# Kernel optimization log

Measured on AMD Instinct MI355X. Metric: run time of the kernel, lower is better.

Reference implementation:

```python
import jax, jax.numpy as jnp
import numpy as np

B, T, C, H = 4, 1024, 2048, 16
D = C // H  # head dim = 128
ALPHA_Q, BETA_Q = -128, 127


def _quant_params(w):
    # symmetric range per tensor, as in get_symmetric_range/get_tensor_quantization_parameters
    beta = float(np.abs(w).max())
    alpha = -beta
    s = (beta - alpha) / (BETA_Q - ALPHA_Q)
    z = int((beta * ALPHA_Q - alpha * BETA_Q) / (beta - alpha))
    return s, z


def _quantize(w, s, z):
    return np.clip(np.round(w / s + z), ALPHA_Q, BETA_Q).astype(np.int8)


def setup_inputs() -> dict:
    key = jax.random.key(0)
    x = jax.random.normal(key, (B, T, C), dtype=jnp.float32)
    rng = np.random.default_rng(0)
    # fp32 master weights (GPT init scale), then quantize per-tensor symmetric int8
    params = {
        'w_attn': rng.normal(0.0, 0.02, (3 * C, C)).astype(np.float32),
        'b_attn': rng.normal(0.0, 0.02, (3 * C,)).astype(np.float32),
        'w_proj': rng.normal(0.0, 0.02, (C, C)).astype(np.float32),
        'b_proj': rng.normal(0.0, 0.02, (C,)).astype(np.float32),
    }
    out = {'x': x}
    for name, arr in params.items():
        s, z = _quant_params(arr)
        out[name + '_q'] = jnp.asarray(_quantize(arr, s, z))
        out['s_' + name] = jnp.float32(s)
        out['z_' + name] = z  # python int, zero-point constant
    return out


def _dequant(wq, s, z):
    # dequantize_tensor: s * (int8 -> int32 - z) -> float32
    return s * (wq.astype(jnp.int32) - z).astype(jnp.float32)


def reference(x, w_attn_q, s_w_attn, z_w_attn, b_attn_q, s_b_attn, z_b_attn,
              w_proj_q, s_w_proj, z_w_proj, b_proj_q, s_b_proj, z_b_proj):
    wa = _dequant(w_attn_q, s_w_attn, z_w_attn)   # [3C, C]
    ba = _dequant(b_attn_q, s_b_attn, z_b_attn)   # [3C]
    wp = _dequant(w_proj_q, s_w_proj, z_w_proj)   # [C, C]
    bp = _dequant(b_proj_q, s_b_proj, z_b_proj)   # [C]

    qkv = jnp.einsum('btc,oc->bto', x, wa) + ba   # [B,T,3C]
    q, k, v = jnp.split(qkv, 3, axis=-1)
    # [B,T,C] -> [B,H,T,D]
    q = q.reshape(B, T, H, D).transpose(0, 2, 1, 3)
    k = k.reshape(B, T, H, D).transpose(0, 2, 1, 3)
    v = v.reshape(B, T, H, D).transpose(0, 2, 1, 3)

    scale = 1.0 / jnp.sqrt(jnp.float32(D))
    scores = jnp.einsum('bhqd,bhkd->bhqk', q, k) * scale  # [B,H,T,T]
    causal = jnp.tril(jnp.ones((T, T), dtype=bool))
    scores = jnp.where(causal, scores, jnp.finfo(scores.dtype).min)
    att = jax.nn.softmax(scores, axis=-1)
    y = jnp.einsum('bhqk,bhkd->bhqd', att, v)      # [B,H,T,D]
    y = y.transpose(0, 2, 1, 3).reshape(B, T, C)

    return jnp.einsum('btc,oc->bto', y, wp) + bp   # [B,T,C]
```

## Files before the change

### kernel.cpp

```cpp
#include <hip/hip_runtime.h>
#include <stdint.h>
#include <math.h>

typedef unsigned short u16;
typedef __attribute__((ext_vector_type(4))) float f32x4;
typedef __attribute__((ext_vector_type(4))) int i32x4;
typedef __attribute__((ext_vector_type(8))) short bf16x8;

__device__ __forceinline__ u16 f2bf(float f) {
  uint32_t u = __float_as_uint(f);
  u += 0x7FFFu + ((u >> 16) & 1u);
  return (u16)(u >> 16);
}

__device__ __forceinline__ void async16(const void* g, void* l) {
  __builtin_amdgcn_global_load_lds(
      (const __attribute__((address_space(1))) void*)g,
      (__attribute__((address_space(3))) void*)l, 16, 0, 0);
}

__global__ void absmax_x(const float4* __restrict__ x, unsigned* __restrict__ amax, int n4) {
  int i = blockIdx.x * 256 + threadIdx.x;
  float m = 0.f;
  for (; i < n4; i += gridDim.x * 256) {
    float4 v = x[i];
    m = fmaxf(m, fmaxf(fmaxf(fabsf(v.x), fabsf(v.y)), fmaxf(fabsf(v.z), fabsf(v.w))));
  }
#pragma unroll
  for (int s = 1; s < 64; s <<= 1) m = fmaxf(m, __shfl_xor(m, s));
  if ((threadIdx.x & 63) == 0) atomicMax(amax, __float_as_uint(m));
}

__global__ void quant_x(const float4* __restrict__ x, char4* __restrict__ o,
                        const unsigned* __restrict__ amax, int n4) {
  int i = blockIdx.x * 256 + threadIdx.x;
  if (i >= n4) return;
  const float inv = 127.0f / __uint_as_float(amax[0]);
  float4 v = x[i];
  char4 r;
  r.x = (char)__float2int_rn(v.x * inv);
  r.y = (char)__float2int_rn(v.y * inv);
  r.z = (char)__float2int_rn(v.z * inv);
  r.w = (char)__float2int_rn(v.w * inv);
  o[i] = r;
}

__global__ void dequant_w8(const int4* __restrict__ q, char4* __restrict__ o, int n4,
                           const int* __restrict__ z) {
  int i = blockIdx.x * 256 + threadIdx.x;
  if (i >= n4) return;
  const int zv = z[0];
  int4 v = q[i];
  char4 r;
  r.x = (char)(v.x - zv); r.y = (char)(v.y - zv);
  r.z = (char)(v.z - zv); r.w = (char)(v.w - zv);
  o[i] = r;
}

__global__ void dequant4(const int4* __restrict__ q, ushort4* __restrict__ o, int n4,
                         const float* __restrict__ s, const int* __restrict__ z) {
  int i = blockIdx.x * 256 + threadIdx.x;
  if (i >= n4) return;
  const float sv = s[0];
  const int zv = z[0];
  int4 v = q[i];
  ushort4 r;
  r.x = f2bf(sv * (float)(v.x - zv));
  r.y = f2bf(sv * (float)(v.y - zv));
  r.z = f2bf(sv * (float)(v.z - zv));
  r.w = f2bf(sv * (float)(v.w - zv));
  o[i] = r;
}

__global__ __launch_bounds__(256, 2) void gemm_i8_qkv(
    const char* __restrict__ A, const char* __restrict__ B, int K,
    const float* __restrict__ sw, const unsigned* __restrict__ amax,
    const int* __restrict__ bq, const float* __restrict__ bs, const int* __restrict__ bz,
    u16* __restrict__ qb, u16* __restrict__ kb, u16* __restrict__ vT) {
  __shared__ uint8_t sA[16384];
  __shared__ uint8_t sB[16384];
  const int tid = threadIdx.x;
  const int wave = tid >> 6, lane = tid & 63;
  const int quad = lane >> 4, l16 = lane & 15;
  const int wm = wave >> 1, wn = wave & 1;
  const int Mb = blockIdx.y << 7, Nb = blockIdx.x << 7;

  const char* ag[4];
  const char* bg[4];
  int lo[4];
#pragma unroll
  for (int i = 0; i < 4; ++i) {
    int row = wave * 32 + i * 8 + (lane >> 3);
    int c = (lane & 7) ^ (row & 7);
    ag[i] = A + (size_t)(Mb + row) * K + c * 16;
    bg[i] = B + (size_t)(Nb + row) * K + c * 16;
    lo[i] = wave * 4096 + i * 1024 + lane * 16;
  }

  i32x4 acc[4][4] = {};

  for (int kk = 0; kk < K; kk += 128) {
    __syncthreads();
#pragma unroll
    for (int i = 0; i < 4; ++i) {
      async16(ag[i] + kk, sA + lo[i]);
      async16(bg[i] + kk, sB + lo[i]);
    }
    __syncthreads();
#pragma unroll
    for (int ks = 0; ks < 2; ++ks) {
      i32x4 af[4], bfr[4];
#pragma unroll
      for (int t = 0; t < 4; ++t) {
        int m = wm * 64 + t * 16 + l16;
        af[t] = *(const i32x4*)(sA + m * 128 + ((((ks << 2) + quad) ^ (m & 7)) << 4));
        int n = wn * 64 + t * 16 + l16;
        bfr[t] = *(const i32x4*)(sB + n * 128 + ((((ks << 2) + quad) ^ (n & 7)) << 4));
      }
#pragma unroll
      for (int mt = 0; mt < 4; ++mt)
#pragma unroll
        for (int nt = 0; nt < 4; ++nt)
          acc[mt][nt] = __builtin_amdgcn_mfma_i32_16x16x64_i8(af[mt], bfr[nt], acc[mt][nt], 0, 0, 0);
    }
  }

  const float sv = sw[0] * (__uint_as_float(amax[0]) / 127.0f);
  const float sbv = bs[0];
  const int zbv = bz[0];
#pragma unroll
  for (int nt = 0; nt < 4; ++nt) {
    const int o = Nb + wn * 64 + nt * 16 + l16;
    const float bias = sbv * (float)(bq[o] - zbv);
    const int which = o >> 11;
    const int cc = o & 2047;
    const int h = cc >> 7, d = cc & 127;
#pragma unroll
    for (int mt = 0; mt < 4; ++mt) {
      const int m0 = Mb + wm * 64 + mt * 16 + quad * 4;
      const int bi = m0 >> 10, t0 = m0 & 1023;
      const size_t bhx = (size_t)bi * 16 + h;
      if (which == 2) {
        ushort4 pv;
        pv.x = f2bf((float)acc[mt][nt][0] * sv + bias);
        pv.y = f2bf((float)acc[mt][nt][1] * sv + bias);
        pv.z = f2bf((float)acc[mt][nt][2] * sv + bias);
        pv.w = f2bf((float)acc[mt][nt][3] * sv + bias);
        *(ushort4*)(vT + (bhx * 128 + d) * 1024 + t0) = pv;
      } else {
        u16* dst = (which == 0 ? qb : kb) + (bhx * 1024 + t0) * 128 + d;
#pragma unroll
        for (int r = 0; r < 4; ++r) dst[r * 128] = f2bf((float)acc[mt][nt][r] * sv + bias);
      }
    }
  }
}

__global__ __launch_bounds__(256, 2) void gemm_bt_out(
    const u16* __restrict__ A, const u16* __restrict__ B, int K, int N,
    const int* __restrict__ bq, const float* __restrict__ bs, const int* __restrict__ bz,
    float* __restrict__ out) {
  __shared__ uint8_t sA[16384];
  __shared__ uint8_t sB[16384];
  const int tid = threadIdx.x;
  const int wave = tid >> 6, lane = tid & 63;
  const int quad = lane >> 4, l16 = lane & 15;
  const int wm = wave >> 1, wn = wave & 1;
  const int Mb = blockIdx.y << 7, Nb = blockIdx.x << 7;

  const u16* ag[4];
  const u16* bg[4];
  int lo[4];
#pragma unroll
  for (int i = 0; i < 4; ++i) {
    int row = wave * 32 + i * 8 + (lane >> 3);
    int c = (lane & 7) ^ (row & 7);
    ag[i] = A + (size_t)(Mb + row) * K + c * 8;
    bg[i] = B + (size_t)(Nb + row) * K + c * 8;
    lo[i] = wave * 4096 + i * 1024 + lane * 16;
  }

  f32x4 acc[4][4] = {};

  for (int kk = 0; kk < K; kk += 64) {
    __syncthreads();
#pragma unroll
    for (int i = 0; i < 4; ++i) {
      async16(ag[i] + kk, sA + lo[i]);
      async16(bg[i] + kk, sB + lo[i]);
    }
    __syncthreads();
#pragma unroll
    for (int ks = 0; ks < 2; ++ks) {
      bf16x8 af[4], bfr[4];
#pragma unroll
      for (int t = 0; t < 4; ++t) {
        int m = wm * 64 + t * 16 + l16;
        af[t] = *(const bf16x8*)(sA + m * 128 + ((((ks << 2) + quad) ^ (m & 7)) << 4));
        int n = wn * 64 + t * 16 + l16;
        bfr[t] = *(const bf16x8*)(sB + n * 128 + ((((ks << 2) + quad) ^ (n & 7)) << 4));
      }
#pragma unroll
      for (int mt = 0; mt < 4; ++mt)
#pragma unroll
        for (int nt = 0; nt < 4; ++nt)
          acc[mt][nt] = __builtin_amdgcn_mfma_f32_16x16x32_bf16(af[mt], bfr[nt], acc[mt][nt], 0, 0, 0);
    }
  }

  const float sbv = bs[0];
  const int zbv = bz[0];
#pragma unroll
  for (int nt = 0; nt < 4; ++nt) {
    const int o = Nb + wn * 64 + nt * 16 + l16;
    const float bias = sbv * (float)(bq[o] - zbv);
#pragma unroll
    for (int mt = 0; mt < 4; ++mt) {
      const int m0 = Mb + wm * 64 + mt * 16 + quad * 4;
#pragma unroll
      for (int r = 0; r < 4; ++r)
        out[(size_t)(m0 + r) * N + o] = acc[mt][nt][r] + bias;
    }
  }
}

__global__ __launch_bounds__(256, 2) void attn_fwd(
    const u16* __restrict__ qg, const u16* __restrict__ kg,
    const u16* __restrict__ vg, u16* __restrict__ yb) {
  __shared__ uint8_t smem[49152];
  uint8_t* sK = smem;
  uint8_t* sV = smem + 16384;
  uint8_t* sP = smem + 32768;
  const int tid = threadIdx.x;
  const int wave = tid >> 6, lane = tid & 63;
  const int quad = lane >> 4, l16 = lane & 15;
  const int bh = blockIdx.x;
  const int y = blockIdx.y;
  const int qi = (y < 4) ? (7 - y) : (y - 4);
  const int qbase = qi << 7;
  const size_t base = (size_t)bh << 17;
  const u16* Q = qg + base;
  const u16* Kp = kg + base;
  const u16* Vp = vg + base;

#pragma unroll
  for (int i = 0; i < 8; ++i) {
    int off = wave * 8192 + i * 1024;
    int row = (off >> 8) + quad;
    int c = l16 ^ (row & 15);
    async16(Q + (size_t)(qbase + row) * 128 + c * 8, smem + off + lane * 16);
  }
  __syncthreads();
  bf16x8 qf[2][4];
#pragma unroll
  for (int mi = 0; mi < 2; ++mi)
#pragma unroll
    for (int ks = 0; ks < 4; ++ks) {
      int m = wave * 32 + mi * 16 + l16;
      qf[mi][ks] = *(const bf16x8*)(smem + m * 256 + ((((ks << 2) + quad) ^ (m & 15)) << 4));
    }

  f32x4 accO[2][8] = {};
  float lacc[2][4] = {};

  const float scale = 0.088388347648318447f;
  const int jmax = 2 * qi + 1;

  for (int j = 0; j <= jmax; ++j) {
    const int tb = j << 6;
    __syncthreads();
#pragma unroll
    for (int i = 0; i < 4; ++i) {
      int off = wave * 4096 + i * 1024;
      int rowk = (off >> 8) + quad;
      int ck = l16 ^ (rowk & 15);
      async16(Kp + (size_t)(tb + rowk) * 128 + ck * 8, sK + off + lane * 16);
      int rowd = (off >> 7) + (lane >> 3);
      int cv = (lane & 7) ^ (rowd & 7);
      async16(Vp + (size_t)rowd * 1024 + tb + cv * 8, sV + off + lane * 16);
    }
    __syncthreads();

    f32x4 sc[2][4] = {};
#pragma unroll
    for (int ks = 0; ks < 4; ++ks) {
      bf16x8 kf[4];
#pragma unroll
      for (int ni = 0; ni < 4; ++ni) {
        int n = ni * 16 + l16;
        kf[ni] = *(const bf16x8*)(sK + n * 256 + ((((ks << 2) + quad) ^ (n & 15)) << 4));
      }
#pragma unroll
      for (int mi = 0; mi < 2; ++mi)
#pragma unroll
        for (int ni = 0; ni < 4; ++ni)
          sc[mi][ni] = __builtin_amdgcn_mfma_f32_16x16x32_bf16(qf[mi][ks], kf[ni], sc[mi][ni], 0, 0, 0);
    }

    const bool needmask = (tb + 63) > qbase;
#pragma unroll
    for (int mi = 0; mi < 2; ++mi) {
      const int row0 = qbase + wave * 32 + mi * 16 + quad * 4;
#pragma unroll
      for (int ni = 0; ni < 4; ++ni) {
        const int col = tb + ni * 16 + l16;
#pragma unroll
        for (int r = 0; r < 4; ++r) {
          float s = sc[mi][ni][r] * scale;
          if (needmask && col > row0 + r) s = -INFINITY;
          float p = __expf(s);
          sc[mi][ni][r] = p;
          lacc[mi][r] += p;
        }
      }
    }

#pragma unroll
    for (int mi = 0; mi < 2; ++mi)
#pragma unroll
      for (int ni = 0; ni < 4; ++ni)
#pragma unroll
        for (int r = 0; r < 4; ++r) {
          int qr = wave * 32 + mi * 16 + quad * 4 + r;
          int kc = ni * 16 + l16;
          *(u16*)(sP + qr * 128 + (((kc >> 3) ^ (qr & 7)) << 4) + (kc & 7) * 2) =
              f2bf(sc[mi][ni][r]);
        }

#pragma unroll
    for (int ks = 0; ks < 2; ++ks) {
      bf16x8 pf[2], vf[8];
#pragma unroll
      for (int mi = 0; mi < 2; ++mi) {
        int m = wave * 32 + mi * 16 + l16;
        pf[mi] = *(const bf16x8*)(sP + m * 128 + ((((ks << 2) + quad) ^ (m & 7)) << 4));
      }
#pragma unroll
      for (int ni = 0; ni < 8; ++ni) {
        int n = ni * 16 + l16;
        vf[ni] = *(const bf16x8*)(sV + n * 128 + ((((ks << 2) + quad) ^ (n & 7)) << 4));
      }
#pragma unroll
      for (int mi = 0; mi < 2; ++mi)
#pragma unroll
        for (int ni = 0; ni < 8; ++ni)
          accO[mi][ni] = __builtin_amdgcn_mfma_f32_16x16x32_bf16(pf[mi], vf[ni], accO[mi][ni], 0, 0, 0);
    }
  }

  const int b = bh >> 4, h = bh & 15;
#pragma unroll
  for (int mi = 0; mi < 2; ++mi) {
    float inv[4];
#pragma unroll
    for (int r = 0; r < 4; ++r) {
      float l = lacc[mi][r];
#pragma unroll
      for (int x = 1; x < 16; x <<= 1) l += __shfl_xor(l, x);
      inv[r] = 1.0f / l;
    }
#pragma unroll
    for (int ni = 0; ni < 8; ++ni)
#pragma unroll
      for (int r = 0; r < 4; ++r) {
        int row = qbase + wave * 32 + mi * 16 + quad * 4 + r;
        int col = (h << 7) + ni * 16 + l16;
        yb[((size_t)(b * 1024 + row) << 11) + col] = f2bf(accO[mi][ni][r] * inv[r]);
      }
  }
}

extern "C" void kernel_launch(void* const* d_in, const int* in_sizes, int n_in,
                              void* d_out, int out_size, void* d_ws, size_t ws_size,
                              hipStream_t stream) {
  const float* x = (const float*)d_in[0];
  const int* waq = (const int*)d_in[1];
  const float* s_wa = (const float*)d_in[2];
  const int* z_wa = (const int*)d_in[3];
  const int* baq = (const int*)d_in[4];
  const float* s_ba = (const float*)d_in[5];
  const int* z_ba = (const int*)d_in[6];
  const int* wpq = (const int*)d_in[7];
  const float* s_wp = (const float*)d_in[8];
  const int* z_wp = (const int*)d_in[9];
  const int* bpq = (const int*)d_in[10];
  const float* s_bp = (const float*)d_in[11];
  const int* z_bp = (const int*)d_in[12];

  char* ws = (char*)d_ws;
  char* xq    = ws + 0;
  char* wa8   = ws + 8388608;
  u16* wp_bf  = (u16*)(ws + 20971520);
  u16* qb     = (u16*)(ws + 29360128);
  u16* kb     = (u16*)(ws + 46137344);
  u16* vT     = (u16*)(ws + 62914560);
  u16* yb     = (u16*)(ws + 79691776);
  unsigned* amax = (unsigned*)(ws + 96468992);

  hipMemsetAsync(amax, 0, 4, stream);
  absmax_x<<<1024, 256, 0, stream>>>((const float4*)x, amax, 2097152);
  quant_x<<<8192, 256, 0, stream>>>((const float4*)x, (char4*)xq, amax, 2097152);
  dequant_w8<<<12288, 256, 0, stream>>>((const int4*)waq, (char4*)wa8, 3145728, z_wa);
  dequant4<<<4096, 256, 0, stream>>>((const int4*)wpq, (ushort4*)wp_bf, 1048576, s_wp, z_wp);

  gemm_i8_qkv<<<dim3(48, 32), 256, 0, stream>>>(xq, wa8, 2048, s_wa, amax,
                                                baq, s_ba, z_ba, qb, kb, vT);

  attn_fwd<<<dim3(64, 8), 256, 0, stream>>>(qb, kb, vT, yb);

  gemm_bt_out<<<dim3(16, 32), 256, 0, stream>>>(yb, wp_bf, 2048, 2048,
                                                bpq, s_bp, z_bp, (float*)d_out);
}
```

Baseline: 338.9 us.

## Rewrite int8 QKV GEMM as 256x256 double-buffered ping-pong pipeline with block swizzle

```diff
diff --git a/kernel.cpp b/kernel.cpp
--- a/kernel.cpp
+++ b/kernel.cpp
@@ -72,85 +72,160 @@
   o[i] = r;
 }
 
-__global__ __launch_bounds__(256, 2) void gemm_i8_qkv(
+
+#define STAGE_A(Q, C, KK, SL) do {                                           \
+    const int row_ = (C)*128 + (Q)*64 + (tid>>3);                            \
+    const int ch_ = (tid&7) ^ (row_&7);                                      \
+    async16(A + (size_t)(Mb + row_)*2048 + (KK) + ch_*16,                    \
+            sA + (SL)*32768 + (C)*16384 + (Q)*8192 + tid*16);                \
+  } while(0)
+
+#define STAGE_B(S, C, KK, SL) do {                                           \
+    const int t8_ = tid & 255, hi_ = tid >> 8;                               \
+    const int row_ = (C)*128 + hi_*64 + (S)*32 + (t8_>>3);                   \
+    const int ch_ = (tid&7) ^ (row_&7);                                      \
+    async16(B + (size_t)(Nb + row_)*2048 + (KK) + ch_*16,                    \
+            sB + (SL)*32768 + (C)*16384 + hi_*8192 + (S)*4096 + t8_*16);     \
+  } while(0)
+
+#define LDA(DST, MQ, SL)                                                     \
+  _Pragma("unroll")                                                          \
+  for (int mp_ = 0; mp_ < 4; ++mp_)                                          \
+    _Pragma("unroll")                                                        \
+    for (int ks_ = 0; ks_ < 2; ++ks_) {                                      \
+      const int r_ = wm*128 + (MQ)*64 + mp_*16 + l16;                        \
+      DST[mp_][ks_] = *(const i32x4*)(sA + (SL)*32768 + r_*128 +             \
+                                      ((((ks_<<2)+quad) ^ (r_&7)) << 4));    \
+    }
+
+#define LDB(DST, NQ, SL)                                                     \
+  _Pragma("unroll")                                                          \
+  for (int np_ = 0; np_ < 2; ++np_)                                          \
+    _Pragma("unroll")                                                        \
+    for (int ks_ = 0; ks_ < 2; ++ks_) {                                      \
+      const int r_ = wn*64 + (NQ)*32 + np_*16 + l16;                         \
+      DST[np_][ks_] = *(const i32x4*)(sB + (SL)*32768 + r_*128 +             \
+                                      ((((ks_<<2)+quad) ^ (r_&7)) << 4));    \
+    }
+
+#define MFMA_QUAD(AF, BF, MQ, NQ)                                            \
+  _Pragma("unroll")                                                          \
+  for (int ks_ = 0; ks_ < 2; ++ks_)                                          \
+    _Pragma("unroll")                                                        \
+    for (int mp_ = 0; mp_ < 4; ++mp_)                                        \
+      _Pragma("unroll")                                                      \
+      for (int np_ = 0; np_ < 2; ++np_)                                      \
+        acc[(MQ)*4+mp_][(NQ)*2+np_] = __builtin_amdgcn_mfma_i32_16x16x64_i8( \
+            AF[mp_][ks_], BF[np_][ks_], acc[(MQ)*4+mp_][(NQ)*2+np_], 0, 0, 0);
+
+#define BARRIER __builtin_amdgcn_s_barrier()
+#define WAIT_LGKM0 do { asm volatile("s_waitcnt lgkmcnt(0)" ::: "memory");   \
+                        __builtin_amdgcn_sched_barrier(0); } while(0)
+#define WAIT_VM8 asm volatile("s_waitcnt vmcnt(8)" ::: "memory")
+
+#define ITER(CUR, NXT, KK2) do {                                             \
+                                                                \
+    STAGE_A(0,0,KK2,CUR); STAGE_A(0,1,KK2,CUR);                              \
+    LDB(b1, 1, CUR);                                                         \
+    BARRIER; WAIT_LGKM0;                                                     \
+    __builtin_amdgcn_s_setprio(1);                                           \
+    MFMA_QUAD(a0, b0, 0, 0);                                                 \
+    __builtin_amdgcn_s_setprio(0);                                           \
+    BARRIER;                                                                 \
+                                                                \
+    LDA(a1, 1, CUR);                                                         \
+    BARRIER; WAIT_LGKM0;                                                     \
+    __builtin_amdgcn_s_setprio(1);                                           \
+    MFMA_QUAD(a0, b1, 0, 1);                                                 \
+    __builtin_amdgcn_s_setprio(0);                                           \
+    BARRIER;                                                                 \
+                                                                \
+    STAGE_A(1,0,KK2,CUR); STAGE_A(1,1,KK2,CUR);                              \
+    STAGE_B(0,0,KK2,CUR); STAGE_B(0,1,KK2,CUR);                              \
+    BARRIER; WAIT_LGKM0;                                                     \
+    __builtin_amdgcn_s_setprio(1);                                           \
+    MFMA_QUAD(a1, b0, 1, 0);                                                 \
+    __builtin_amdgcn_s_setprio(0);                                           \
+    WAIT_VM8;                                                                \
+    BARRIER;                                                                 \
+                                                                \
+    STAGE_B(1,0,KK2,CUR); STAGE_B(1,1,KK2,CUR);                              \
+    LDA(a0, 0, NXT); LDB(b0, 0, NXT);                                        \
+    BARRIER; WAIT_LGKM0;                                                     \
+    __builtin_amdgcn_s_setprio(1);                                           \
+    MFMA_QUAD(a1, b1, 1, 1);                                                 \
+    __builtin_amdgcn_s_setprio(0);                                           \
+    WAIT_VM8;                                                                \
+    BARRIER;                                                                 \
+  } while(0)
+
+__global__ __launch_bounds__(512, 2) void gemm_i8_qkv(
     const char* __restrict__ A, const char* __restrict__ B, int K,
     const float* __restrict__ sw, const unsigned* __restrict__ amax,
     const int* __restrict__ bq, const float* __restrict__ bs, const int* __restrict__ bz,
     u16* __restrict__ qb, u16* __restrict__ kb, u16* __restrict__ vT) {
-  __shared__ uint8_t sA[16384];
-  __shared__ uint8_t sB[16384];
+  __shared__ uint8_t sA[65536];
+  __shared__ uint8_t sB[65536];
   const int tid = threadIdx.x;
   const int wave = tid >> 6, lane = tid & 63;
   const int quad = lane >> 4, l16 = lane & 15;
-  const int wm = wave >> 1, wn = wave & 1;
-  const int Mb = blockIdx.y << 7, Nb = blockIdx.x << 7;
-
-  const char* ag[4];
-  const char* bg[4];
-  int lo[4];
-#pragma unroll
-  for (int i = 0; i < 4; ++i) {
-    int row = wave * 32 + i * 8 + (lane >> 3);
-    int c = (lane & 7) ^ (row & 7);
-    ag[i] = A + (size_t)(Mb + row) * K + c * 16;
-    bg[i] = B + (size_t)(Nb + row) * K + c * 16;
-    lo[i] = wave * 4096 + i * 1024 + lane * 16;
-  }
-
-  i32x4 acc[4][4] = {};
-
-  for (int kk = 0; kk < K; kk += 128) {
-    __syncthreads();
-#pragma unroll
-    for (int i = 0; i < 4; ++i) {
-      async16(ag[i] + kk, sA + lo[i]);
-      async16(bg[i] + kk, sB + lo[i]);
-    }
-    __syncthreads();
-#pragma unroll
-    for (int ks = 0; ks < 2; ++ks) {
-      i32x4 af[4], bfr[4];
-#pragma unroll
-      for (int t = 0; t < 4; ++t) {
-        int m = wm * 64 + t * 16 + l16;
-        af[t] = *(const i32x4*)(sA + m * 128 + ((((ks << 2) + quad) ^ (m & 7)) << 4));
-        int n = wn * 64 + t * 16 + l16;
-        bfr[t] = *(const i32x4*)(sB + n * 128 + ((((ks << 2) + quad) ^ (n & 7)) << 4));
-      }
-#pragma unroll
-      for (int mt = 0; mt < 4; ++mt)
-#pragma unroll
-        for (int nt = 0; nt < 4; ++nt)
-          acc[mt][nt] = __builtin_amdgcn_mfma_i32_16x16x64_i8(af[mt], bfr[nt], acc[mt][nt], 0, 0, 0);
-    }
-  }
+  const int wm = wave >> 2, wn = wave & 3;
+
+  const int bid = blockIdx.y * 24 + blockIdx.x;
+  const int swz = (bid & 7) * 48 + (bid >> 3);
+  const int Nb = (swz % 24) << 8;
+  const int Mb = (swz / 24) << 8;
+
+  i32x4 acc[8][4] = {};
+  i32x4 a0[4][2], a1[4][2];
+  i32x4 b0[2][2], b1[2][2];
+
+  STAGE_A(0,0,0,0); STAGE_A(0,1,0,0); STAGE_A(1,0,0,0); STAGE_A(1,1,0,0);
+  STAGE_B(0,0,0,0); STAGE_B(0,1,0,0); STAGE_B(1,0,0,0); STAGE_B(1,1,0,0);
+  STAGE_A(0,0,128,1); STAGE_A(0,1,128,1); STAGE_A(1,0,128,1); STAGE_A(1,1,128,1);
+  STAGE_B(0,0,128,1); STAGE_B(0,1,128,1); STAGE_B(1,0,128,1); STAGE_B(1,1,128,1);
+  WAIT_VM8;
+  BARRIER;
+  LDA(a0, 0, 0); LDB(b0, 0, 0);
+  WAIT_LGKM0;
+  BARRIER;
+
+#pragma unroll 1
+  for (int T2 = 0; T2 < 8; ++T2) {
+    const int ta = 2 * T2 + 2, tb = 2 * T2 + 3;
+    const int kka = (ta < 16 ? ta : 15) << 7;
+    const int kkb = (tb < 16 ? tb : 15) << 7;
+    ITER(0, 1, kka);
+    ITER(1, 0, kkb);
+  }
+  asm volatile("s_waitcnt vmcnt(0)" ::: "memory");
 
   const float sv = sw[0] * (__uint_as_float(amax[0]) / 127.0f);
   const float sbv = bs[0];
   const int zbv = bz[0];
 #pragma unroll
-  for (int nt = 0; nt < 4; ++nt) {
-    const int o = Nb + wn * 64 + nt * 16 + l16;
+  for (int nn = 0; nn < 4; ++nn) {
+    const int o = Nb + wn * 64 + nn * 16 + l16;
     const float bias = sbv * (float)(bq[o] - zbv);
     const int which = o >> 11;
     const int cc = o & 2047;
     const int h = cc >> 7, d = cc & 127;
 #pragma unroll
-    for (int mt = 0; mt < 4; ++mt) {
-      const int m0 = Mb + wm * 64 + mt * 16 + quad * 4;
+    for (int mm = 0; mm < 8; ++mm) {
+      const int m0 = Mb + wm * 128 + mm * 16 + quad * 4;
       const int bi = m0 >> 10, t0 = m0 & 1023;
       const size_t bhx = (size_t)bi * 16 + h;
       if (which == 2) {
         ushort4 pv;
-        pv.x = f2bf((float)acc[mt][nt][0] * sv + bias);
-        pv.y = f2bf((float)acc[mt][nt][1] * sv + bias);
-        pv.z = f2bf((float)acc[mt][nt][2] * sv + bias);
-        pv.w = f2bf((float)acc[mt][nt][3] * sv + bias);
+        pv.x = f2bf((float)acc[mm][nn][0] * sv + bias);
+        pv.y = f2bf((float)acc[mm][nn][1] * sv + bias);
+        pv.z = f2bf((float)acc[mm][nn][2] * sv + bias);
+        pv.w = f2bf((float)acc[mm][nn][3] * sv + bias);
         *(ushort4*)(vT + (bhx * 128 + d) * 1024 + t0) = pv;
       } else {
         u16* dst = (which == 0 ? qb : kb) + (bhx * 1024 + t0) * 128 + d;
 #pragma unroll
-        for (int r = 0; r < 4; ++r) dst[r * 128] = f2bf((float)acc[mt][nt][r] * sv + bias);
+        for (int r = 0; r < 4; ++r) dst[r * 128] = f2bf((float)acc[mm][nn][r] * sv + bias);
       }
     }
   }
@@ -403,7 +478,7 @@
   dequant_w8<<<12288, 256, 0, stream>>>((const int4*)waq, (char4*)wa8, 3145728, z_wa);
   dequant4<<<4096, 256, 0, stream>>>((const int4*)wpq, (ushort4*)wp_bf, 1048576, s_wp, z_wp);
 
-  gemm_i8_qkv<<<dim3(48, 32), 256, 0, stream>>>(xq, wa8, 2048, s_wa, amax,
+  gemm_i8_qkv<<<dim3(24, 16), 512, 0, stream>>>(xq, wa8, 2048, s_wa, amax,
                                                 baq, s_ba, z_ba, qb, kb, vT);
 
   attn_fwd<<<dim3(64, 8), 256, 0, stream>>>(qb, kb, vT, yb);
```

Result: slower. 371.0 us (+9.5%).

## Triple-buffer the int8 QKV GEMM with async LDS loads and a wider tile

Applied to the files above, without the earlier changes.

```diff
diff --git a/kernel.cpp b/kernel.cpp
--- a/kernel.cpp
+++ b/kernel.cpp
@@ -72,58 +72,86 @@
   o[i] = r;
 }
 
-__global__ __launch_bounds__(256, 2) void gemm_i8_qkv(
-    const char* __restrict__ A, const char* __restrict__ B, int K,
+
+#define QSTAGE_A(KK, SL) do {                                                \
+    _Pragma("unroll")                                                        \
+    for (int c_ = 0; c_ < 2; ++c_) {                                         \
+      const int row_ = c_*64 + (tid>>3);                                     \
+      const int ch_ = (tid&7) ^ (row_&7);                                    \
+      async16(A + (size_t)(Mb + row_)*2048 + (KK) + ch_*16,                  \
+              sA + (SL)*16384 + c_*8192 + tid*16);                           \
+    }                                                                        \
+  } while(0)
+
+#define QSTAGE_B(KK, SL) do {                                                \
+    _Pragma("unroll")                                                        \
+    for (int c_ = 0; c_ < 4; ++c_) {                                         \
+      const int row_ = c_*64 + (tid>>3);                                     \
+      const int ch_ = (tid&7) ^ (row_&7);                                    \
+      async16(Bm + (size_t)(Nb + row_)*2048 + (KK) + ch_*16,                 \
+              sB + (SL)*32768 + c_*8192 + tid*16);                           \
+    }                                                                        \
+  } while(0)
+
+__global__ __launch_bounds__(512, 2) void gemm_i8_qkv(
+    const char* __restrict__ A, const char* __restrict__ Bm, int K,
     const float* __restrict__ sw, const unsigned* __restrict__ amax,
     const int* __restrict__ bq, const float* __restrict__ bs, const int* __restrict__ bz,
     u16* __restrict__ qb, u16* __restrict__ kb, u16* __restrict__ vT) {
-  __shared__ uint8_t sA[16384];
-  __shared__ uint8_t sB[16384];
+  __shared__ uint8_t sA[49152];
+  __shared__ uint8_t sB[98304];
   const int tid = threadIdx.x;
   const int wave = tid >> 6, lane = tid & 63;
   const int quad = lane >> 4, l16 = lane & 15;
-  const int wm = wave >> 1, wn = wave & 1;
-  const int Mb = blockIdx.y << 7, Nb = blockIdx.x << 7;
-
-  const char* ag[4];
-  const char* bg[4];
-  int lo[4];
-#pragma unroll
-  for (int i = 0; i < 4; ++i) {
-    int row = wave * 32 + i * 8 + (lane >> 3);
-    int c = (lane & 7) ^ (row & 7);
-    ag[i] = A + (size_t)(Mb + row) * K + c * 16;
-    bg[i] = B + (size_t)(Nb + row) * K + c * 16;
-    lo[i] = wave * 4096 + i * 1024 + lane * 16;
-  }
+  const int wm = wave >> 2, wn = wave & 3;
+  const int Mb = blockIdx.y << 7, Nb = blockIdx.x << 8;
 
   i32x4 acc[4][4] = {};
 
-  for (int kk = 0; kk < K; kk += 128) {
-    __syncthreads();
-#pragma unroll
-    for (int i = 0; i < 4; ++i) {
-      async16(ag[i] + kk, sA + lo[i]);
-      async16(bg[i] + kk, sB + lo[i]);
-    }
-    __syncthreads();
-#pragma unroll
-    for (int ks = 0; ks < 2; ++ks) {
-      i32x4 af[4], bfr[4];
-#pragma unroll
-      for (int t = 0; t < 4; ++t) {
-        int m = wm * 64 + t * 16 + l16;
-        af[t] = *(const i32x4*)(sA + m * 128 + ((((ks << 2) + quad) ^ (m & 7)) << 4));
-        int n = wn * 64 + t * 16 + l16;
-        bfr[t] = *(const i32x4*)(sB + n * 128 + ((((ks << 2) + quad) ^ (n & 7)) << 4));
-      }
+  QSTAGE_A(0, 0); QSTAGE_B(0, 0);
+  QSTAGE_A(128, 1); QSTAGE_B(128, 1);
+  asm volatile("s_waitcnt vmcnt(6)" ::: "memory");
+  __builtin_amdgcn_s_barrier();
+
+  int slr = 0, slw = 2;
+#pragma unroll 1
+  for (int t = 0; t < 16; ++t) {
+    const int kst = (t + 2 < 16 ? t + 2 : 15) << 7;
+    QSTAGE_A(kst, slw); QSTAGE_B(kst, slw);
+
+    i32x4 af[4][2], bf[4][2];
+#pragma unroll
+    for (int mt = 0; mt < 4; ++mt)
+#pragma unroll
+      for (int ks = 0; ks < 2; ++ks) {
+        const int r = wm * 64 + mt * 16 + l16;
+        af[mt][ks] = *(const i32x4*)(sA + slr * 16384 + r * 128 +
+                                     ((((ks << 2) + quad) ^ (r & 7)) << 4));
+      }
+#pragma unroll
+    for (int nt = 0; nt < 4; ++nt)
+#pragma unroll
+      for (int ks = 0; ks < 2; ++ks) {
+        const int r = wn * 64 + nt * 16 + l16;
+        bf[nt][ks] = *(const i32x4*)(sB + slr * 32768 + r * 128 +
+                                     ((((ks << 2) + quad) ^ (r & 7)) << 4));
+      }
+    asm volatile("s_waitcnt lgkmcnt(0)" ::: "memory");
+    __builtin_amdgcn_sched_barrier(0);
+#pragma unroll
+    for (int ks = 0; ks < 2; ++ks)
 #pragma unroll
       for (int mt = 0; mt < 4; ++mt)
 #pragma unroll
         for (int nt = 0; nt < 4; ++nt)
-          acc[mt][nt] = __builtin_amdgcn_mfma_i32_16x16x64_i8(af[mt], bfr[nt], acc[mt][nt], 0, 0, 0);
-    }
-  }
+          acc[mt][nt] = __builtin_amdgcn_mfma_i32_16x16x64_i8(af[mt][ks], bf[nt][ks],
+                                                              acc[mt][nt], 0, 0, 0);
+    asm volatile("s_waitcnt vmcnt(6)" ::: "memory");
+    __builtin_amdgcn_s_barrier();
+    slr = (slr == 2) ? 0 : slr + 1;
+    slw = (slw == 2) ? 0 : slw + 1;
+  }
+  asm volatile("s_waitcnt vmcnt(0)" ::: "memory");
 
   const float sv = sw[0] * (__uint_as_float(amax[0]) / 127.0f);
   const float sbv = bs[0];
@@ -403,7 +431,7 @@
   dequant_w8<<<12288, 256, 0, stream>>>((const int4*)waq, (char4*)wa8, 3145728, z_wa);
   dequant4<<<4096, 256, 0, stream>>>((const int4*)wpq, (ushort4*)wp_bf, 1048576, s_wp, z_wp);
 
-  gemm_i8_qkv<<<dim3(48, 32), 256, 0, stream>>>(xq, wa8, 2048, s_wa, amax,
+  gemm_i8_qkv<<<dim3(24, 32), 512, 0, stream>>>(xq, wa8, 2048, s_wa, amax,
                                                 baq, s_ba, z_ba, qb, kb, vT);
 
   attn_fwd<<<dim3(64, 8), 256, 0, stream>>>(qb, kb, vT, yb);
```

New measurement: 358.1 us. +5.6%, slower.

## Double-buffer K/V tiles in attention with async prefetch of next block

Applied to the files above, without the earlier changes.

```diff
diff --git a/kernel.cpp b/kernel.cpp
--- a/kernel.cpp
+++ b/kernel.cpp
@@ -227,10 +227,9 @@
 __global__ __launch_bounds__(256, 2) void attn_fwd(
     const u16* __restrict__ qg, const u16* __restrict__ kg,
     const u16* __restrict__ vg, u16* __restrict__ yb) {
-  __shared__ uint8_t smem[49152];
-  uint8_t* sK = smem;
-  uint8_t* sV = smem + 16384;
-  uint8_t* sP = smem + 32768;
+  __shared__ uint8_t smem[81920];
+  uint8_t* sVb = smem + 32768;
+  uint8_t* sP = smem + 65536;
   const int tid = threadIdx.x;
   const int wave = tid >> 6, lane = tid & 63;
   const int quad = lane >> 4, l16 = lane & 15;
@@ -259,6 +258,24 @@
       int m = wave * 32 + mi * 16 + l16;
       qf[mi][ks] = *(const bf16x8*)(smem + m * 256 + ((((ks << 2) + quad) ^ (m & 15)) << 4));
     }
+  asm volatile("s_waitcnt lgkmcnt(0)" ::: "memory");
+  __builtin_amdgcn_sched_barrier(0);
+  __builtin_amdgcn_s_barrier();
+
+#define STAGEKV(TB, SL) do {                                                  \
+    _Pragma("unroll")                                                         \
+    for (int i_ = 0; i_ < 4; ++i_) {                                          \
+      int off_ = wave * 4096 + i_ * 1024;                                     \
+      int rowk_ = (off_ >> 8) + quad;                                         \
+      int ck_ = l16 ^ (rowk_ & 15);                                           \
+      async16(Kp + (size_t)((TB) + rowk_) * 128 + ck_ * 8,                    \
+              smem + (SL) * 16384 + off_ + lane * 16);                        \
+      int rowd_ = (off_ >> 7) + (lane >> 3);                                  \
+      int cv_ = (lane & 7) ^ (rowd_ & 7);                                     \
+      async16(Vp + (size_t)rowd_ * 1024 + (TB) + cv_ * 8,                     \
+              sVb + (SL) * 16384 + off_ + lane * 16);                         \
+    }                                                                         \
+  } while (0)
 
   f32x4 accO[2][8] = {};
   float lacc[2][4] = {};
@@ -266,20 +283,16 @@
   const float scale = 0.088388347648318447f;
   const int jmax = 2 * qi + 1;
 
+  STAGEKV(0, 0);
+
   for (int j = 0; j <= jmax; ++j) {
     const int tb = j << 6;
-    __syncthreads();
-#pragma unroll
-    for (int i = 0; i < 4; ++i) {
-      int off = wave * 4096 + i * 1024;
-      int rowk = (off >> 8) + quad;
-      int ck = l16 ^ (rowk & 15);
-      async16(Kp + (size_t)(tb + rowk) * 128 + ck * 8, sK + off + lane * 16);
-      int rowd = (off >> 7) + (lane >> 3);
-      int cv = (lane & 7) ^ (rowd & 7);
-      async16(Vp + (size_t)rowd * 1024 + tb + cv * 8, sV + off + lane * 16);
-    }
-    __syncthreads();
+    const int jn = (j + 1 <= jmax) ? j + 1 : jmax;
+    STAGEKV(jn << 6, (j + 1) & 1);
+    asm volatile("s_waitcnt vmcnt(8)" ::: "memory");
+    __builtin_amdgcn_s_barrier();
+    const uint8_t* sK = smem + (j & 1) * 16384;
+    const uint8_t* sV = sVb + (j & 1) * 16384;
 
     f32x4 sc[2][4] = {};
 #pragma unroll
@@ -346,7 +359,9 @@
         for (int ni = 0; ni < 8; ++ni)
           accO[mi][ni] = __builtin_amdgcn_mfma_f32_16x16x32_bf16(pf[mi], vf[ni], accO[mi][ni], 0, 0, 0);
     }
-  }
+    __builtin_amdgcn_s_barrier();
+  }
+  asm volatile("s_waitcnt vmcnt(0)" ::: "memory");
 
   const int b = bh >> 4, h = bh & 15;
 #pragma unroll
@@ -368,6 +383,7 @@
         yb[((size_t)(b * 1024 + row) << 11) + col] = f2bf(accO[mi][ni][r] * inv[r]);
       }
   }
+#undef STAGEKV
 }
 
 extern "C" void kernel_launch(void* const* d_in, const int* in_sizes, int n_in,
```

New measurement: 340.6 us. About the same (+0.5%).
